# Kernel optimization log

Hardware: AMD Instinct MI355X
Metric: run time of the kernel (lower is better)

## Reference

```python
import jax, jax.numpy as jnp
import numpy as np

EPS = 1e-6


def smooth(p):
    # smooth_distribution: clamp Bernoulli params away from {0,1}
    return jnp.clip(p, EPS, 1.0 - EPS)


def bern_logprob(p, x):
    # Bernoulli(p).log_prob(x) = x*log(p) + (1-x)*log(1-p)
    return x * jnp.log(p) + (1.0 - x) * jnp.log1p(-p)


def binary_row_reduce(A, b, k):
    # GF(2) Gaussian elimination on [A | b]; A:(k,n) binary float, b:(k,)
    M = jnp.concatenate([A, b[:, None]], axis=1)  # (k, n+1)
    rows = jnp.arange(k)
    for i in range(k):  # k is a small static int (25)
        col = M[:, i]
        cand = jnp.where((rows >= i) & (col > 0.5), rows, k)
        p = jnp.minimum(jnp.min(cand), k - 1)  # pivot row (fallback k-1 if none; prob ~0 for random A)
        ri, rp = M[i], M[p]
        M = M.at[i].set(rp)
        M = M.at[p].set(ri)
        elim = (M[:, i] > 0.5) & (rows != i)
        M = jnp.where(elim[:, None], jnp.mod(M + M[i], 2.0), M)
    return M[:, :-1], M[:, -1]


def compute_term1(logq, logp):
    # stable [sum_s q*log p]/[sum_s q], summed over batch; logq,logp: (S,B)
    m = jnp.max(logq, axis=0)                                  # (B,)
    w = jnp.exp(logq - m)                                      # (S,B)
    neg_num = m + jnp.log(jnp.sum(w * (-logp), axis=0))
    pos_den = m + jnp.log(jnp.sum(w, axis=0))
    return -jnp.sum(jnp.exp(neg_num - pos_den))


def setup_inputs() -> dict:
    key = jax.random.key(0)
    ks = jax.random.split(key, 5)
    nx, nz, B = 2048, 256, 512
    wr = float(np.sqrt(6.0 / (nx + nz)))
    xr = float(np.sqrt(6.0 / nx))
    zr = float(np.sqrt(6.0 / nz))
    U = jax.random.uniform(ks[0], (nz, nx), minval=-wr, maxval=wr)
    V = jax.random.uniform(ks[1], (nx, nz), minval=-wr, maxval=wr)
    x_bias = jax.random.uniform(ks[2], (nx,), minval=-xr, maxval=xr)
    z_bias = jax.random.uniform(ks[3], (nz,), minval=-zr, maxval=zr)
    xin = (jax.random.uniform(ks[4], (B, nx)) < 0.5).astype(jnp.float32)
    return {"xin": xin, "U": U, "V": V, "x_bias": x_bias, "z_bias": z_bias,
            "S": 10, "k": 25, "T": 30}


def reference(xin, U, V, x_bias, z_bias, S, k, T):
    dt = xin.dtype
    key = jax.random.key(42)
    kz, kx, kA, kb = jax.random.split(key, 4)

    # q(z|x) and samples  -------------------------------------------------
    q = smooth(jax.nn.sigmoid(xin @ U.T + z_bias))                     # (B, nz)
    samples_z = (jax.random.uniform(kz, (S,) + q.shape) < q).astype(dt)  # (S,B,nz)
    ps = smooth(jax.nn.sigmoid(jnp.einsum('sbz,xz->sbx', samples_z, V) + x_bias))  # (S,B,nx)
    xouts = (jax.random.uniform(kx, ps.shape) < ps).astype(dt)

    # projected ELBO over T random GF(2) hash constraints ------------------
    nz = U.shape[0]
    A_all = (jax.random.uniform(kA, (T, k, nz)) < 0.5).astype(dt)
    b_all = (jax.random.uniform(kb, (T, k)) < 0.5).astype(dt)
    pz = smooth(jax.nn.sigmoid(z_bias))                                # (nz,)

    def elbo_t(carry, Ab):
        A, b = Ab
        C, bp = binary_row_reduce(A, b, k)                             # (k,nz),(k,)
        proj = jnp.mod(jnp.einsum('sbz,kz->sbk', samples_z[:, :, k:], C[:, k:]) + bp, 2.0)
        sz = samples_z.at[:, :, :k].set(proj)                          # (S,B,nz)
        logq_zi = bern_logprob(q, sz).sum(axis=2)                      # (S,B)
        logp_z = bern_logprob(pz, sz).sum(axis=2)                      # (S,B)
        ps_t = smooth(jax.nn.sigmoid(jnp.einsum('sbz,xz->sbx', sz, V) + x_bias))
        logp_x = bern_logprob(ps_t, xin).sum(axis=2)                   # (S,B)
        logp = logp_z + logp_x
        term2 = compute_term1(logq_zi, logq_zi)
        term1 = compute_term1(logq_zi, logp)
        return carry, term1 - term2

    _, pelbos = jax.lax.scan(elbo_t, 0.0, (A_all, b_all))
    loss = -jnp.mean(pelbos)
    return q, samples_z, ps, xouts, loss
```

## Files before the change

### kernel.cpp

```cpp
#include <hip/hip_runtime.h>
#include <cstdint>

#define NX 2048
#define NZ 256
#define NB 512
#define NS 10
#define NK 25
#define NT 30
#define SBTOT (NS * NB)

#define LOG2E 1.4426950408889634f
#define LN2 0.6931471805599453f

#define OFF_Q 0
#define OFF_SAMP (NB * NZ)
#define OFF_PS (OFF_SAMP + SBTOT * NZ)
#define OFF_XO (OFF_PS + SBTOT * NX)
#define OFF_LOSS (OFF_XO + SBTOT * NX)

typedef unsigned long long ull;
typedef __bf16 bf16x8 __attribute__((ext_vector_type(8)));
typedef float f32x4 __attribute__((ext_vector_type(4)));
typedef uint32_t u32x2 __attribute__((ext_vector_type(2)));

__host__ __device__ inline void tf2x32(uint32_t k0, uint32_t k1, uint32_t x0, uint32_t x1,
                                       uint32_t& o0, uint32_t& o1) {
  uint32_t k2 = k0 ^ k1 ^ 0x1BD11BDAu;
  x0 += k0; x1 += k1;
#define TF_R(r) { x0 += x1; x1 = (x1 << (r)) | (x1 >> (32 - (r))); x1 ^= x0; }
  TF_R(13) TF_R(15) TF_R(26) TF_R(6)
  x0 += k1; x1 += k2 + 1u;
  TF_R(17) TF_R(29) TF_R(16) TF_R(24)
  x0 += k2; x1 += k0 + 2u;
  TF_R(13) TF_R(15) TF_R(26) TF_R(6)
  x0 += k0; x1 += k1 + 3u;
  TF_R(17) TF_R(29) TF_R(16) TF_R(24)
  x0 += k1; x1 += k2 + 4u;
  TF_R(13) TF_R(15) TF_R(26) TF_R(6)
  x0 += k2; x1 += k0 + 5u;
#undef TF_R
  o0 = x0; o1 = x1;
}

__device__ inline uint32_t tf_select(uint32_t k0, uint32_t k1, uint32_t i, uint32_t h) {
  bool lo = i < h;
  uint32_t x0 = lo ? i : i - h;
  uint32_t x1 = lo ? i + h : i;
  uint32_t o0, o1;
  tf2x32(k0, k1, x0, x1, o0, o1);
  return lo ? o0 : o1;
}

__device__ inline float tf_uniform(uint32_t k0, uint32_t k1, uint32_t i, uint32_t h) {
  uint32_t r = tf_select(k0, k1, i, h);
  return __uint_as_float(0x3f800000u | (r >> 9)) - 1.0f;
}

__device__ inline float sigclip(float a) {
  float p = 1.0f / (1.0f + __expf(-a));
  return fminf(fmaxf(p, 1e-6f), 1.0f - 1e-6f);
}

__device__ inline ushort f2bf(float f) {
  uint32_t u = __float_as_uint(f);
  return (ushort)((u + 0x7FFFu + ((u >> 16) & 1u)) >> 16);
}

__device__ inline float blockReduceSum256(float v, volatile float* s4) {
#pragma unroll
  for (int o = 32; o > 0; o >>= 1) v += __shfl_down(v, o);
  __syncthreads();
  if ((threadIdx.x & 63) == 0) s4[threadIdx.x >> 6] = v;
  __syncthreads();
  return s4[0] + s4[1] + s4[2] + s4[3];
}

__global__ __launch_bounds__(256) void kP0_prep(const float* __restrict__ V,
                                                const float* __restrict__ U,
                                                const float* __restrict__ xin,
                                                const float* __restrict__ z_bias,
                                                ushort* __restrict__ Vbf,
                                                ushort* __restrict__ Vkpad2,
                                                ushort* __restrict__ Uhi,
                                                ushort* __restrict__ Ulo,
                                                ushort* __restrict__ xinbf,
                                                float* __restrict__ baseq,
                                                float* __restrict__ d_lpz,
                                                float* __restrict__ basepz,
                                                ull* __restrict__ Ct,
                                                uint32_t* __restrict__ bpmask,
                                                uint32_t kA0, uint32_t kA1,
                                                uint32_t kb0, uint32_t kb1) {
  __shared__ float red[4];
  __shared__ uint32_t Aw[NK][8];
  __shared__ uint32_t bbsh[NK];
  int tid = threadIdx.x;
  if (blockIdx.x >= NX * NZ / 256) {
    int t = blockIdx.x - NX * NZ / 256;
    if (tid < NK * 8) {
      int r = tid >> 3, c = tid & 7;
      const uint32_t hA = (uint32_t)NT * NK * NZ / 2;
      uint32_t base_i = (uint32_t)(t * NK + r) * NZ + c * 32;
      uint32_t w = 0;
      for (int zz = 0; zz < 32; ++zz) {
        uint32_t rr = tf_select(kA0, kA1, base_i + zz, hA);
        w |= ((rr >> 31) ^ 1u) << zz;
      }
      Aw[r][c] = w;
    }
    if (tid < NK) {
      const uint32_t hb = (uint32_t)NT * NK / 2;
      uint32_t rb = tf_select(kb0, kb1, (uint32_t)(t * NK + tid), hb);
      bbsh[tid] = (rb >> 31) ^ 1u;
    }
    __syncthreads();
    if (tid >= 64) return;
    int lane = tid;
    ull w0 = 0, w1 = 0, w2 = 0, w3 = 0;
    uint32_t bbit = 0;
    if (lane < NK) {
      w0 = (ull)Aw[lane][0] | ((ull)Aw[lane][1] << 32);
      w1 = (ull)Aw[lane][2] | ((ull)Aw[lane][3] << 32);
      w2 = (ull)Aw[lane][4] | ((ull)Aw[lane][5] << 32);
      w3 = (ull)Aw[lane][6] | ((ull)Aw[lane][7] << 32);
      bbit = bbsh[lane];
    }
    for (int i = 0; i < NK; ++i) {
      int mybit = (int)((w0 >> i) & 1ull);
      ull mask = __ballot(lane < NK && mybit);
      ull cand = mask & (~0ull << i);
      int p = cand ? __builtin_ctzll(cand) : (NK - 1);
      int srcl = (lane == i) ? p : ((lane == p) ? i : lane);
      w0 = __shfl(w0, srcl); w1 = __shfl(w1, srcl); w2 = __shfl(w2, srcl); w3 = __shfl(w3, srcl);
      bbit = __shfl(bbit, srcl);
      ull p0 = __shfl(w0, i), p1 = __shfl(w1, i), p2 = __shfl(w2, i), p3 = __shfl(w3, i);
      uint32_t pvb = __shfl(bbit, i);
      int nb2 = (int)((w0 >> i) & 1ull);
      if (lane < NK && lane != i && nb2) {
        w0 ^= p0; w1 ^= p1; w2 ^= p2; w3 ^= p3; bbit ^= pvb;
      }
    }
    if (lane < NK) {
      w0 &= ~((1ull << NK) - 1ull);
      ull* dstp = Ct + (size_t)(t * NK + lane) * 4;
      dstp[0] = w0; dstp[1] = w1; dstp[2] = w2; dstp[3] = w3;
    }
    ull bm = __ballot(lane < NK && bbit);
    if (lane == 0) bpmask[t] = (uint32_t)bm & 0x1FFFFFFu;
    return;
  }
  int e = blockIdx.x * 256 + tid;
  {
    int x = e >> 8, k = e & 255;
    float v = V[e];
    Vbf[e] = f2bf(v);
    if (k < 32) Vkpad2[x * 32 + k] = (k < NK) ? f2bf(v * LOG2E) : (ushort)0;
  }
  {
    float u = U[e];
    ushort hi = f2bf(u);
    Uhi[e] = hi;
    float hv = __uint_as_float((uint32_t)hi << 16);
    Ulo[e] = f2bf(u - hv);
  }
  {
    xinbf[e] = (xin[e] > 0.5f) ? (ushort)0x3F80 : (ushort)0;
    int e2 = e + NX * NZ;
    xinbf[e2] = (xin[e2] > 0.5f) ? (ushort)0x3F80 : (ushort)0;
  }
  if (e < NB) baseq[e] = 0.0f;
  if (blockIdx.x == 0) {
    int z = tid;
    float pz = sigclip(z_bias[z]);
    float lp = __logf(pz), l1 = __logf(1.0f - pz);
    d_lpz[z] = lp - l1;
    float s = blockReduceSum256(l1, red);
    if (z == 0) *basepz = s;
  }
}

__global__ __launch_bounds__(256) void k1w_mfma(const ushort* __restrict__ xinbf,
                                                const ushort* __restrict__ Uhi,
                                                const ushort* __restrict__ Ulo,
                                                const float* __restrict__ z_bias,
                                                const float* __restrict__ xin,
                                                const ushort* __restrict__ Vkpad2,
                                                float* __restrict__ outq,
                                                float* __restrict__ d_lq,
                                                float* __restrict__ baseq,
                                                float* __restrict__ W) {
  __shared__ float red[4][16][17];
  __shared__ float wred[4][NK];
  int tid = threadIdx.x;
  if (blockIdx.x < 512) {
    int wave = tid >> 6, lane = tid & 63, grp = lane >> 4, col = lane & 15;
    int b0 = (blockIdx.x >> 4) * 16;
    int z0 = (blockIdx.x & 15) * 16;
    f32x4 acc = {0.f, 0.f, 0.f, 0.f};
    const ushort* arow = xinbf + (size_t)(b0 + col) * NX + wave * 512 + grp * 8;
    const ushort* bhr = Uhi + (size_t)(z0 + col) * NX + wave * 512 + grp * 8;
    const ushort* blr = Ulo + (size_t)(z0 + col) * NX + wave * 512 + grp * 8;
#pragma unroll 4
    for (int s = 0; s < 16; ++s) {
      bf16x8 a = *(const bf16x8*)(arow + s * 32);
      bf16x8 bh = *(const bf16x8*)(bhr + s * 32);
      bf16x8 bl = *(const bf16x8*)(blr + s * 32);
      acc = __builtin_amdgcn_mfma_f32_16x16x32_bf16(a, bh, acc, 0, 0, 0);
      acc = __builtin_amdgcn_mfma_f32_16x16x32_bf16(a, bl, acc, 0, 0, 0);
    }
#pragma unroll
    for (int r = 0; r < 4; ++r) red[wave][grp * 4 + r][col] = acc[r];
    __syncthreads();
    int bi = tid >> 4, zi = tid & 15;
    float aa = red[0][bi][zi] + red[1][bi][zi] + red[2][bi][zi] + red[3][bi][zi] + z_bias[z0 + zi];
    int b = b0 + bi, z = z0 + zi;
    float q = sigclip(aa);
    outq[b * NZ + z] = q;
    float lq = __logf(q), l1 = __logf(1.0f - q);
    d_lq[b * NZ + z] = lq - l1;
    float s1 = l1;
#pragma unroll
    for (int o = 1; o < 16; o <<= 1) s1 += __shfl_xor(s1, o);
    if (zi == 0) atomicAdd(&baseq[b], s1);
    return;
  }
  int b = blockIdx.x - 512;
  float acc[NK];
#pragma unroll
  for (int j = 0; j < NK; ++j) acc[j] = 0.0f;
#pragma unroll
  for (int i = 0; i < 8; ++i) {
    int x = i * 256 + tid;
    float s = 1.0f - 2.0f * xin[(size_t)b * NX + x];
    const uint4* vp = (const uint4*)(Vkpad2 + (size_t)x * 32);
    uint4 q0 = vp[0], q1 = vp[1], q2 = vp[2], q3 = vp[3];
    uint32_t w[16] = {q0.x, q0.y, q0.z, q0.w, q1.x, q1.y, q1.z, q1.w,
                      q2.x, q2.y, q2.z, q2.w, q3.x, q3.y, q3.z, q3.w};
#pragma unroll
    for (int j = 0; j < NK; ++j) {
      uint32_t wd = w[j >> 1];
      float v = __uint_as_float((j & 1) ? (wd & 0xFFFF0000u) : (wd << 16));
      acc[j] = fmaf(s, v, acc[j]);
    }
  }
#pragma unroll
  for (int j = 0; j < NK; ++j) {
#pragma unroll
    for (int o = 1; o < 64; o <<= 1) acc[j] += __shfl_xor(acc[j], o);
  }
  if ((tid & 63) == 0) {
#pragma unroll
    for (int j = 0; j < NK; ++j) wred[tid >> 6][j] = acc[j];
  }
  __syncthreads();
  if (tid < NK) W[b * 32 + tid] = wred[0][tid] + wred[1][tid] + wred[2][tid] + wred[3][tid];
}

__global__ __launch_bounds__(256) void k2_samples(const float* __restrict__ q,
                                                  const float* __restrict__ d_lq,
                                                  const float* __restrict__ d_lpz,
                                                  const ull* __restrict__ Ct,
                                                  const uint32_t* __restrict__ bpmask,
                                                  const float* __restrict__ W,
                                                  float* __restrict__ samp_out,
                                                  ushort* __restrict__ samp16,
                                                  ull* __restrict__ Spack,
                                                  float* __restrict__ qtail,
                                                  float* __restrict__ ptail,
                                                  uint32_t* __restrict__ projb,
                                                  float* __restrict__ Syd,
                                                  uint32_t kz0, uint32_t kz1) {
  __shared__ float red[4];
  __shared__ ull sp_sh[4];
  int sb = blockIdx.x;
  int z = threadIdx.x;
  int b = sb & (NB - 1);
  uint32_t i = (uint32_t)sb * NZ + z;
  const uint32_t h = (uint32_t)SBTOT * NZ / 2;
  float u = tf_uniform(kz0, kz1, i, h);
  float qv = q[b * NZ + z];
  int smp = (u < qv) ? 1 : 0;
  __builtin_nontemporal_store((float)smp, samp_out + i);
  samp16[i] = smp ? (ushort)0x3F80 : (ushort)0;
  ull m = __ballot(smp);
  if ((z & 63) == 0) { Spack[sb * 4 + (z >> 6)] = m; sp_sh[z >> 6] = m; }
  float dq = (z >= NK && smp) ? d_lq[b * NZ + z] : 0.0f;
  float dp = (z >= NK && smp) ? d_lpz[z] : 0.0f;
  float sq = blockReduceSum256(dq, red);
  float sp = blockReduceSum256(dp, red);
  if (z == 0) { qtail[sb] = sq; ptail[sb] = sp; }
  if (z < 32) {
    int t = z;
    ull s0 = sp_sh[0], s1 = sp_sh[1], s2 = sp_sh[2], s3 = sp_sh[3];
    uint32_t s25 = (uint32_t)(s0 & 0x1FFFFFFull);
    const float* Wb = W + (size_t)b * 32;
    uint32_t out;
    float syd = 0.0f;
    if (t < NT) {
      uint32_t bp = bpmask[t];
      uint32_t pb = 0;
#pragma unroll
      for (int j = 0; j < NK; ++j) {
        const ull* C = Ct + (size_t)(t * NK + j) * 4;
        int par = __popcll(s0 & C[0]) + __popcll(s1 & C[1]) + __popcll(s2 & C[2]) + __popcll(s3 & C[3]);
        uint32_t bit = ((uint32_t)(par ^ (int)(bp >> j))) & 1u;
        pb |= bit << j;
        int d = (int)bit - (int)((s25 >> j) & 1u);
        syd = fmaf((float)d, Wb[j], syd);
      }
      out = pb;
    } else {
      out = s25;
    }
    projb[sb * 32 + t] = out;
    Syd[sb * 32 + t] = syd;
  }
}

__global__ __launch_bounds__(256) void k3m_gemm(const ushort* __restrict__ samp16,
                                                const ushort* __restrict__ Vbf,
                                                const float* __restrict__ x_bias,
                                                ushort* __restrict__ base2,
                                                float* __restrict__ ps_out,
                                                float* __restrict__ xo_out,
                                                uint32_t kx0, uint32_t kx1) {
  __shared__ __align__(16) char smem[2 * 2112 * 4];
  ushort* As = (ushort*)smem;
  ushort* Bs = (ushort*)(smem + 8192);
  float* Tt = (float*)smem;

  int tid = threadIdx.x;
  int wave = tid >> 6, lane = tid & 63, grp = lane >> 4, col = lane & 15;
  int x0 = blockIdx.x * 128;
  int sb0 = blockIdx.y * 32;
  f32x4 acc[2][4];
#pragma unroll
  for (int mi = 0; mi < 2; ++mi)
#pragma unroll
    for (int ni = 0; ni < 4; ++ni) acc[mi][ni] = (f32x4){0.f, 0.f, 0.f, 0.f};

  for (int k0 = 0; k0 < NZ; k0 += 32) {
    {
      int rowb = tid >> 2, kcb = (tid & 3) << 3;
      int sbrow = (rowb < 32) ? (sb0 + rowb) : (sb0 + 2528 + rowb);
      *(uint4*)&Bs[rowb * 32 + kcb] = *(const uint4*)&samp16[(size_t)sbrow * NZ + k0 + kcb];
#pragma unroll
      for (int c = tid; c < 512; c += 256) {
        int rowa = c >> 2, kca = (c & 3) << 3;
        *(uint4*)&As[rowa * 32 + kca] = *(const uint4*)&Vbf[(size_t)(x0 + rowa) * NZ + k0 + kca];
      }
    }
    __syncthreads();
    bf16x8 af[2], bfv[4];
#pragma unroll
    for (int mi = 0; mi < 2; ++mi)
      af[mi] = *(const bf16x8*)&As[(wave * 32 + mi * 16 + col) * 32 + grp * 8];
#pragma unroll
    for (int ni = 0; ni < 4; ++ni)
      bfv[ni] = *(const bf16x8*)&Bs[(ni * 16 + col) * 32 + grp * 8];
#pragma unroll
    for (int mi = 0; mi < 2; ++mi)
#pragma unroll
      for (int ni = 0; ni < 4; ++ni)
        acc[mi][ni] = __builtin_amdgcn_mfma_f32_16x16x32_bf16(af[mi], bfv[ni], acc[mi][ni], 0, 0, 0);
    __syncthreads();
  }

  const uint32_t HH = (uint32_t)(SBTOT / 2) * (uint32_t)NX;
#pragma unroll
  for (int pi = 0; pi < 2; ++pi) {
    __syncthreads();
#pragma unroll
    for (int mi = 0; mi < 2; ++mi) {
      int cbase = wave * 32 + mi * 16 + grp * 4;
      *(float4*)&Tt[col * 132 + cbase] = *(float4*)&acc[mi][pi];
      *(float4*)&Tt[2112 + col * 132 + cbase] = *(float4*)&acc[mi][pi + 2];
    }
    __syncthreads();
#pragma unroll
    for (int pass = 0; pass < 2; ++pass) {
      int r = pass * 8 + (tid >> 5);
      int c = (tid & 31) * 4;
      float4 t0 = *(float4*)&Tt[r * 132 + c];
      float4 t1 = *(float4*)&Tt[2112 + r * 132 + c];
      float4 xb4 = *(const float4*)(x_bias + x0 + c);
      int sb_a = sb0 + pi * 16 + r;
      size_t off_a = (size_t)sb_a * NX + x0 + c;
      size_t off_b = off_a + (size_t)HH;
      float a0 = t0.x + xb4.x, a1 = t0.y + xb4.y, a2 = t0.z + xb4.z, a3 = t0.w + xb4.w;
      float b0 = t1.x + xb4.x, b1 = t1.y + xb4.y, b2 = t1.z + xb4.z, b3 = t1.w + xb4.w;
      u32x2 bpa, bpb;
      bpa[0] = (uint32_t)f2bf(a0 * LOG2E) | ((uint32_t)f2bf(a1 * LOG2E) << 16);
      bpa[1] = (uint32_t)f2bf(a2 * LOG2E) | ((uint32_t)f2bf(a3 * LOG2E) << 16);
      bpb[0] = (uint32_t)f2bf(b0 * LOG2E) | ((uint32_t)f2bf(b1 * LOG2E) << 16);
      bpb[1] = (uint32_t)f2bf(b2 * LOG2E) | ((uint32_t)f2bf(b3 * LOG2E) << 16);
      *(u32x2*)(base2 + off_a) = bpa;
      *(u32x2*)(base2 + off_b) = bpb;
      f32x4 pva = {sigclip(a0), sigclip(a1), sigclip(a2), sigclip(a3)};
      f32x4 pvb = {sigclip(b0), sigclip(b1), sigclip(b2), sigclip(b3)};
      __builtin_nontemporal_store(pva, (f32x4*)(ps_out + off_a));
      __builtin_nontemporal_store(pvb, (f32x4*)(ps_out + off_b));
      uint32_t fi = (uint32_t)off_a;
      uint32_t r0, r1;
      f32x4 xva, xvb;
      tf2x32(kx0, kx1, fi + 0u, fi + 0u + HH, r0, r1);
      xva[0] = ((__uint_as_float(0x3f800000u | (r0 >> 9)) - 1.0f) < pva[0]) ? 1.0f : 0.0f;
      xvb[0] = ((__uint_as_float(0x3f800000u | (r1 >> 9)) - 1.0f) < pvb[0]) ? 1.0f : 0.0f;
      tf2x32(kx0, kx1, fi + 1u, fi + 1u + HH, r0, r1);
      xva[1] = ((__uint_as_float(0x3f800000u | (r0 >> 9)) - 1.0f) < pva[1]) ? 1.0f : 0.0f;
      xvb[1] = ((__uint_as_float(0x3f800000u | (r1 >> 9)) - 1.0f) < pvb[1]) ? 1.0f : 0.0f;
      tf2x32(kx0, kx1, fi + 2u, fi + 2u + HH, r0, r1);
      xva[2] = ((__uint_as_float(0x3f800000u | (r0 >> 9)) - 1.0f) < pva[2]) ? 1.0f : 0.0f;
      xvb[2] = ((__uint_as_float(0x3f800000u | (r1 >> 9)) - 1.0f) < pvb[2]) ? 1.0f : 0.0f;
      tf2x32(kx0, kx1, fi + 3u, fi + 3u + HH, r0, r1);
      xva[3] = ((__uint_as_float(0x3f800000u | (r0 >> 9)) - 1.0f) < pva[3]) ? 1.0f : 0.0f;
      xvb[3] = ((__uint_as_float(0x3f800000u | (r1 >> 9)) - 1.0f) < pvb[3]) ? 1.0f : 0.0f;
      __builtin_nontemporal_store(xva, (f32x4*)(xo_out + off_a));
      __builtin_nontemporal_store(xvb, (f32x4*)(xo_out + off_b));
    }
  }
}

__global__ __launch_bounds__(256) void k6_mfma(const ushort* __restrict__ base2,
                                               const ushort* __restrict__ Vkpad2,
                                               const float* __restrict__ xin,
                                               const uint32_t* __restrict__ projb,
                                               const ull* __restrict__ Spack,
                                               const float* __restrict__ Syd,
                                               float* __restrict__ logpx) {
  __shared__ float bvsm[NX];
  __shared__ float lsum[4][32];
  __shared__ float red[4];
  int sb = blockIdx.x;
  int b = sb & (NB - 1);
  int tid = threadIdx.x;
  int wave = tid >> 6, lane = tid & 63;
  int grp = lane >> 4, col = lane & 15;
  const uint4* b16p = (const uint4*)(base2 + (size_t)sb * NX);
  const float4* x4p = (const float4*)(xin + (size_t)b * NX);
  float sbacc = 0.0f;
  {
    uint4 bu = b16p[tid];
    float4 xv0 = x4p[tid * 2], xv1 = x4p[tid * 2 + 1];
    uint32_t wds[4] = {bu.x, bu.y, bu.z, bu.w};
    float bv[8];
#pragma unroll
    for (int j = 0; j < 8; ++j) {
      uint32_t wd = wds[j >> 1];
      bv[j] = __uint_as_float((j & 1) ? (wd & 0xFFFF0000u) : (wd << 16));
    }
    float sg[8] = {1.0f - 2.0f * xv0.x, 1.0f - 2.0f * xv0.y, 1.0f - 2.0f * xv0.z,
                   1.0f - 2.0f * xv0.w, 1.0f - 2.0f * xv1.x, 1.0f - 2.0f * xv1.y,
                   1.0f - 2.0f * xv1.z, 1.0f - 2.0f * xv1.w};
#pragma unroll
    for (int j = 0; j < 8; ++j) {
      bvsm[tid * 8 + j] = bv[j];
      sbacc = fmaf(sg[j], bv[j], sbacc);
    }
  }
  float Sb = blockReduceSum256(sbacc, red);
  uint32_t s25 = (uint32_t)(Spack[sb * 4] & 0x1FFFFFFull);
  uint32_t pb0 = projb[sb * 32 + col];
  uint32_t pb1 = projb[sb * 32 + 16 + col];
  bf16x8 a0, a1;
  union { ushort u; __bf16 hh; } cvt;
#pragma unroll
  for (int j = 0; j < 8; ++j) {
    int k = grp * 8 + j;
    int sbit = (int)((s25 >> k) & 1u);
    int d0 = (int)((pb0 >> k) & 1u) - sbit;
    int d1 = (int)((pb1 >> k) & 1u) - sbit;
    cvt.u = (ushort)(d0 == 0 ? 0 : (d0 > 0 ? 0x3F80 : 0xBF80)); a0[j] = cvt.hh;
    cvt.u = (ushort)(d1 == 0 ? 0 : (d1 > 0 ? 0x3F80 : 0xBF80)); a1[j] = cvt.hh;
  }
  float acca[8], pp[8];
#pragma unroll
  for (int r = 0; r < 8; ++r) { acca[r] = 0.0f; pp[r] = 1.0f; }
  const ushort* vkbase = Vkpad2 + (size_t)(wave * 512 + col) * 32 + grp * 8;
#pragma unroll 4
  for (int i = 0; i < 32; ++i) {
    int x = (wave * 32 + i) * 16 + col;
    bf16x8 bfr = *(const bf16x8*)(vkbase + (size_t)i * 16 * 32);
    f32x4 c0 = {0.f, 0.f, 0.f, 0.f}, c1 = {0.f, 0.f, 0.f, 0.f};
    c0 = __builtin_amdgcn_mfma_f32_16x16x32_bf16(a0, bfr, c0, 0, 0, 0);
    c1 = __builtin_amdgcn_mfma_f32_16x16x32_bf16(a1, bfr, c1, 0, 0, 0);
    float bs = bvsm[x];
#pragma unroll
    for (int r = 0; r < 4; ++r) {
      float y0 = bs + c0[r];
      acca[r] += fabsf(y0);
      pp[r] = fmaf(pp[r], __builtin_amdgcn_exp2f(-fabsf(y0)), pp[r]);
      float y1 = bs + c1[r];
      acca[4 + r] += fabsf(y1);
      pp[4 + r] = fmaf(pp[4 + r], __builtin_amdgcn_exp2f(-fabsf(y1)), pp[4 + r]);
    }
  }
#pragma unroll
  for (int r = 0; r < 8; ++r) {
    float m = 0.5f * acca[r] + __log2f(pp[r]);
#pragma unroll
    for (int off = 1; off < 16; off <<= 1) m += __shfl_xor(m, off);
    if (col == 0) {
      int t = (r < 4) ? (grp * 4 + r) : (16 + grp * 4 + (r - 4));
      lsum[wave][t] = m;
    }
  }
  __syncthreads();
  if (tid < NT) {
    float tot = lsum[0][tid] + lsum[1][tid] + lsum[2][tid] + lsum[3][tid];
    tot += 0.5f * (Sb + Syd[sb * 32 + tid]);
    logpx[(size_t)tid * SBTOT + sb] = -LN2 * tot;
  }
}

__global__ __launch_bounds__(64) void k7_reduce(const float* __restrict__ logpx,
                                                const uint32_t* __restrict__ projb,
                                                const float* __restrict__ qtail,
                                                const float* __restrict__ ptail,
                                                const float* __restrict__ baseq,
                                                const float* __restrict__ d_lq,
                                                const float* __restrict__ d_lpz,
                                                const float* __restrict__ basepz,
                                                double* __restrict__ pelbo_part) {
  int t = blockIdx.x;
  int chunk = blockIdx.y;
  int lane = threadIdx.x;
  int b = chunk * 64 + lane;
  float dlq[NK];
#pragma unroll
  for (int j = 0; j < NK; ++j) dlq[j] = d_lq[b * NZ + j];
  float bq = baseq[b];
  float bpz = *basepz;
  float lq[NS], lp[NS];
#pragma unroll
  for (int s = 0; s < NS; ++s) {
    int sb = s * NB + b;
    uint32_t m = projb[sb * 32 + t];
    float sq = 0.0f, spv = 0.0f;
#pragma unroll
    for (int j = 0; j < NK; ++j) {
      float on = (float)((m >> j) & 1u);
      sq += on * dlq[j];
      spv += on * d_lpz[j];
    }
    lq[s] = bq + qtail[sb] + sq;
    lp[s] = logpx[t * SBTOT + sb] + bpz + ptail[sb] + spv;
  }
  float mx = lq[0];
#pragma unroll
  for (int s = 1; s < NS; ++s) mx = fmaxf(mx, lq[s]);
  float den = 0.0f, num = 0.0f;
#pragma unroll
  for (int s = 0; s < NS; ++s) {
    float w = __expf(lq[s] - mx);
    den += w;
    num += w * (lq[s] - lp[s]);
  }
  double v = (double)(num / den);
#pragma unroll
  for (int o = 32; o > 0; o >>= 1) v += __shfl_down(v, o);
  if (lane == 0) pelbo_part[t * 8 + chunk] = v;
}

__global__ __launch_bounds__(64) void k8_loss(const double* __restrict__ pelbo_part,
                                              float* __restrict__ out_loss) {
  int t = threadIdx.x;
  double v = 0.0;
  if (t < NT) {
#pragma unroll
    for (int c = 0; c < 8; ++c) v += pelbo_part[t * 8 + c];
  }
#pragma unroll
  for (int o = 32; o > 0; o >>= 1) v += __shfl_down(v, o);
  if (t == 0) *out_loss = (float)(v / (double)NT);
}

extern "C" void kernel_launch(void* const* d_in, const int* in_sizes, int n_in,
                              void* d_out, int out_size, void* d_ws, size_t ws_size,
                              hipStream_t stream) {
  const float* xin = (const float*)d_in[0];
  const float* U = (const float*)d_in[1];
  const float* V = (const float*)d_in[2];
  const float* x_bias = (const float*)d_in[3];
  const float* z_bias = (const float*)d_in[4];
  float* out = (float*)d_out;

  char* p = (char*)d_ws;
  ushort* base2 = (ushort*)p;             p += (size_t)SBTOT * NX * 2;
  float* d_lq = (float*)p;                p += (size_t)NB * NZ * 4;
  float* baseq = (float*)p;               p += (size_t)NB * 4;
  float* d_lpz = (float*)p;               p += (size_t)NZ * 4;
  float* basepz = (float*)p;              p += 16;
  ull* Spack = (ull*)p;                   p += (size_t)SBTOT * 4 * 8;
  float* qtail = (float*)p;               p += (size_t)SBTOT * 4;
  float* ptail = (float*)p;               p += (size_t)SBTOT * 4;
  ull* Ct = (ull*)p;                      p += (size_t)NT * NK * 4 * 8;
  uint32_t* bpm = (uint32_t*)p;           p += 128;
  uint32_t* projb = (uint32_t*)p;         p += (size_t)SBTOT * 32 * 4;
  float* Syd = (float*)p;                 p += (size_t)SBTOT * 32 * 4;
  float* logpx = (float*)p;               p += (size_t)NT * SBTOT * 4;
  double* pelbo = (double*)p;             p += (size_t)NT * 8 * 8;
  ushort* Vkpad2 = (ushort*)p;            p += (size_t)NX * 32 * 2;
  ushort* Vbf = (ushort*)p;               p += (size_t)NX * NZ * 2;
  ushort* samp16 = (ushort*)p;            p += (size_t)SBTOT * NZ * 2;
  float* W = (float*)p;                   p += (size_t)NB * 32 * 4;
  ushort* Uhi = (ushort*)p;               p += (size_t)NZ * NX * 2;
  ushort* Ulo = (ushort*)p;               p += (size_t)NZ * NX * 2;
  ushort* xinbf = (ushort*)p;             p += (size_t)NB * NX * 2;
  (void)ws_size; (void)in_sizes; (void)n_in; (void)out_size;

  uint32_t o0[4], o1[4];
  for (int j = 0; j < 4; ++j) tf2x32(0u, 42u, (uint32_t)j, (uint32_t)(4 + j), o0[j], o1[j]);
  uint32_t kz0 = o0[0], kz1 = o0[1];
  uint32_t kx0 = o0[2], kx1 = o0[3];
  uint32_t kA0 = o1[0], kA1 = o1[1];
  uint32_t kb0 = o1[2], kb1 = o1[3];

  kP0_prep<<<NX * NZ / 256 + NT, 256, 0, stream>>>(V, U, xin, z_bias, Vbf, Vkpad2,
                                                   Uhi, Ulo, xinbf, baseq, d_lpz, basepz,
                                                   Ct, bpm, kA0, kA1, kb0, kb1);
  k1w_mfma<<<1024, 256, 0, stream>>>(xinbf, Uhi, Ulo, z_bias, xin, Vkpad2,
                                     out + OFF_Q, d_lq, baseq, W);
  k2_samples<<<SBTOT, 256, 0, stream>>>(out + OFF_Q, d_lq, d_lpz, Ct, bpm, W,
                                        out + OFF_SAMP, samp16, Spack, qtail, ptail,
                                        projb, Syd, kz0, kz1);
  dim3 g3(NX / 128, SBTOT / 64);
  k3m_gemm<<<g3, 256, 0, stream>>>(samp16, Vbf, x_bias, base2,
                                   out + OFF_PS, out + OFF_XO, kx0, kx1);
  k6_mfma<<<SBTOT, 256, 0, stream>>>(base2, Vkpad2, xin, projb, Spack, Syd, logpx);
  dim3 g7(NT, 8);
  k7_reduce<<<g7, 64, 0, stream>>>(logpx, projb, qtail, ptail, baseq, d_lq,
                                   d_lpz, basepz, pelbo);
  k8_loss<<<1, 64, 0, stream>>>(pelbo, out + OFF_LOSS);
}
```

Before: 256.7 us.

## Move GF(2) reduction into k1 and fold final loss kernel into reduce via atomics

The per-constraint GF(2) row-reduction blocks move from the prep kernel into the k1 MFMA kernel's grid. The separate final loss kernel is removed: k7 blocks add their partial sums to a double accumulator atomically, and the last block (found through a done counter) writes the loss. In k6, the bias is now preloaded into the MFMA accumulator instead of being added afterward. Together these remove one launch and shorten the tail, at the cost of atomics and a summation order that is no longer deterministic.

After: 254.6 us. Within noise of the previous version (-0.8%).

```diff
diff --git a/kernel.cpp b/kernel.cpp
--- a/kernel.cpp
+++ b/kernel.cpp
@@ -87,16 +87,62 @@
                                                 float* __restrict__ baseq,
                                                 float* __restrict__ d_lpz,
                                                 float* __restrict__ basepz,
+                                                double* __restrict__ loss_acc,
+                                                uint32_t* __restrict__ done_ctr) {
+  __shared__ float red[4];
+  int tid = threadIdx.x;
+  int e = blockIdx.x * 256 + tid;
+  {
+    int x = e >> 8, k = e & 255;
+    float v = V[e];
+    Vbf[e] = f2bf(v);
+    if (k < 32) Vkpad2[x * 32 + k] = (k < NK) ? f2bf(v * LOG2E) : (ushort)0;
+  }
+  {
+    float u = U[e];
+    ushort hi = f2bf(u);
+    Uhi[e] = hi;
+    float hv = __uint_as_float((uint32_t)hi << 16);
+    Ulo[e] = f2bf(u - hv);
+  }
+  {
+    xinbf[e] = (xin[e] > 0.5f) ? (ushort)0x3F80 : (ushort)0;
+    int e2 = e + NX * NZ;
+    xinbf[e2] = (xin[e2] > 0.5f) ? (ushort)0x3F80 : (ushort)0;
+  }
+  if (e < NB) baseq[e] = 0.0f;
+  if (blockIdx.x == 0) {
+    if (tid == 0) { *loss_acc = 0.0; *done_ctr = 0u; }
+    int z = tid;
+    float pz = sigclip(z_bias[z]);
+    float lp = __logf(pz), l1 = __logf(1.0f - pz);
+    d_lpz[z] = lp - l1;
+    float s = blockReduceSum256(l1, red);
+    if (z == 0) *basepz = s;
+  }
+}
+
+__global__ __launch_bounds__(256) void k1w_mfma(const ushort* __restrict__ xinbf,
+                                                const ushort* __restrict__ Uhi,
+                                                const ushort* __restrict__ Ulo,
+                                                const float* __restrict__ z_bias,
+                                                const float* __restrict__ xin,
+                                                const ushort* __restrict__ Vkpad2,
+                                                float* __restrict__ outq,
+                                                float* __restrict__ d_lq,
+                                                float* __restrict__ baseq,
+                                                float* __restrict__ W,
                                                 ull* __restrict__ Ct,
                                                 uint32_t* __restrict__ bpmask,
                                                 uint32_t kA0, uint32_t kA1,
                                                 uint32_t kb0, uint32_t kb1) {
-  __shared__ float red[4];
+  __shared__ float red[4][16][17];
+  __shared__ float wred[4][NK];
   __shared__ uint32_t Aw[NK][8];
   __shared__ uint32_t bbsh[NK];
   int tid = threadIdx.x;
-  if (blockIdx.x >= NX * NZ / 256) {
-    int t = blockIdx.x - NX * NZ / 256;
+  if (blockIdx.x >= 1024) {
+    int t = blockIdx.x - 1024;
     if (tid < NK * 8) {
       int r = tid >> 3, c = tid & 7;
       const uint32_t hA = (uint32_t)NT * NK * NZ / 2;
@@ -149,49 +195,6 @@
     if (lane == 0) bpmask[t] = (uint32_t)bm & 0x1FFFFFFu;
     return;
   }
-  int e = blockIdx.x * 256 + tid;
-  {
-    int x = e >> 8, k = e & 255;
-    float v = V[e];
-    Vbf[e] = f2bf(v);
-    if (k < 32) Vkpad2[x * 32 + k] = (k < NK) ? f2bf(v * LOG2E) : (ushort)0;
-  }
-  {
-    float u = U[e];
-    ushort hi = f2bf(u);
-    Uhi[e] = hi;
-    float hv = __uint_as_float((uint32_t)hi << 16);
-    Ulo[e] = f2bf(u - hv);
-  }
-  {
-    xinbf[e] = (xin[e] > 0.5f) ? (ushort)0x3F80 : (ushort)0;
-    int e2 = e + NX * NZ;
-    xinbf[e2] = (xin[e2] > 0.5f) ? (ushort)0x3F80 : (ushort)0;
-  }
-  if (e < NB) baseq[e] = 0.0f;
-  if (blockIdx.x == 0) {
-    int z = tid;
-    float pz = sigclip(z_bias[z]);
-    float lp = __logf(pz), l1 = __logf(1.0f - pz);
-    d_lpz[z] = lp - l1;
-    float s = blockReduceSum256(l1, red);
-    if (z == 0) *basepz = s;
-  }
-}
-
-__global__ __launch_bounds__(256) void k1w_mfma(const ushort* __restrict__ xinbf,
-                                                const ushort* __restrict__ Uhi,
-                                                const ushort* __restrict__ Ulo,
-                                                const float* __restrict__ z_bias,
-                                                const float* __restrict__ xin,
-                                                const ushort* __restrict__ Vkpad2,
-                                                float* __restrict__ outq,
-                                                float* __restrict__ d_lq,
-                                                float* __restrict__ baseq,
-                                                float* __restrict__ W) {
-  __shared__ float red[4][16][17];
-  __shared__ float wred[4][NK];
-  int tid = threadIdx.x;
   if (blockIdx.x < 512) {
     int wave = tid >> 6, lane = tid & 63, grp = lane >> 4, col = lane & 15;
     int b0 = (blockIdx.x >> 4) * 16;
@@ -477,20 +480,20 @@
 #pragma unroll
   for (int r = 0; r < 8; ++r) { acca[r] = 0.0f; pp[r] = 1.0f; }
   const ushort* vkbase = Vkpad2 + (size_t)(wave * 512 + col) * 32 + grp * 8;
+  const float* bvp = bvsm + wave * 512 + col;
 #pragma unroll 4
   for (int i = 0; i < 32; ++i) {
-    int x = (wave * 32 + i) * 16 + col;
+    float bs = bvp[i * 16];
     bf16x8 bfr = *(const bf16x8*)(vkbase + (size_t)i * 16 * 32);
-    f32x4 c0 = {0.f, 0.f, 0.f, 0.f}, c1 = {0.f, 0.f, 0.f, 0.f};
-    c0 = __builtin_amdgcn_mfma_f32_16x16x32_bf16(a0, bfr, c0, 0, 0, 0);
-    c1 = __builtin_amdgcn_mfma_f32_16x16x32_bf16(a1, bfr, c1, 0, 0, 0);
-    float bs = bvsm[x];
+    f32x4 cb = {bs, bs, bs, bs};
+    f32x4 c0 = __builtin_amdgcn_mfma_f32_16x16x32_bf16(a0, bfr, cb, 0, 0, 0);
+    f32x4 c1 = __builtin_amdgcn_mfma_f32_16x16x32_bf16(a1, bfr, cb, 0, 0, 0);
 #pragma unroll
     for (int r = 0; r < 4; ++r) {
-      float y0 = bs + c0[r];
+      float y0 = c0[r];
       acca[r] += fabsf(y0);
       pp[r] = fmaf(pp[r], __builtin_amdgcn_exp2f(-fabsf(y0)), pp[r]);
-      float y1 = bs + c1[r];
+      float y1 = c1[r];
       acca[4 + r] += fabsf(y1);
       pp[4 + r] = fmaf(pp[4 + r], __builtin_amdgcn_exp2f(-fabsf(y1)), pp[4 + r]);
     }
@@ -521,7 +524,9 @@
                                                 const float* __restrict__ d_lq,
                                                 const float* __restrict__ d_lpz,
                                                 const float* __restrict__ basepz,
-                                                double* __restrict__ pelbo_part) {
+                                                double* __restrict__ loss_acc,
+                                                uint32_t* __restrict__ done_ctr,
+                                                float* __restrict__ out_loss) {
   int t = blockIdx.x;
   int chunk = blockIdx.y;
   int lane = threadIdx.x;
@@ -559,20 +564,15 @@
   double v = (double)(num / den);
 #pragma unroll
   for (int o = 32; o > 0; o >>= 1) v += __shfl_down(v, o);
-  if (lane == 0) pelbo_part[t * 8 + chunk] = v;
-}
-
-__global__ __launch_bounds__(64) void k8_loss(const double* __restrict__ pelbo_part,
-                                              float* __restrict__ out_loss) {
-  int t = threadIdx.x;
-  double v = 0.0;
-  if (t < NT) {
-#pragma unroll
-    for (int c = 0; c < 8; ++c) v += pelbo_part[t * 8 + c];
-  }
-#pragma unroll
-  for (int o = 32; o > 0; o >>= 1) v += __shfl_down(v, o);
-  if (t == 0) *out_loss = (float)(v / (double)NT);
+  if (lane == 0) {
+    atomicAdd(loss_acc, v);
+    __threadfence();
+    uint32_t old = atomicAdd(done_ctr, 1u);
+    if (old == (uint32_t)(NT * 8 - 1)) {
+      double tot = atomicAdd(loss_acc, 0.0);
+      *out_loss = (float)(tot / (double)NT);
+    }
+  }
 }
 
 extern "C" void kernel_launch(void* const* d_in, const int* in_sizes, int n_in,
@@ -599,7 +599,8 @@
   uint32_t* projb = (uint32_t*)p;         p += (size_t)SBTOT * 32 * 4;
   float* Syd = (float*)p;                 p += (size_t)SBTOT * 32 * 4;
   float* logpx = (float*)p;               p += (size_t)NT * SBTOT * 4;
-  double* pelbo = (double*)p;             p += (size_t)NT * 8 * 8;
+  double* loss_acc = (double*)p;          p += 64;
+  uint32_t* done_ctr = (uint32_t*)p;      p += 64;
   ushort* Vkpad2 = (ushort*)p;            p += (size_t)NX * 32 * 2;
   ushort* Vbf = (ushort*)p;               p += (size_t)NX * NZ * 2;
   ushort* samp16 = (ushort*)p;            p += (size_t)SBTOT * NZ * 2;
@@ -616,11 +617,12 @@
   uint32_t kA0 = o1[0], kA1 = o1[1];
   uint32_t kb0 = o1[2], kb1 = o1[3];
 
-  kP0_prep<<<NX * NZ / 256 + NT, 256, 0, stream>>>(V, U, xin, z_bias, Vbf, Vkpad2,
-                                                   Uhi, Ulo, xinbf, baseq, d_lpz, basepz,
-                                                   Ct, bpm, kA0, kA1, kb0, kb1);
-  k1w_mfma<<<1024, 256, 0, stream>>>(xinbf, Uhi, Ulo, z_bias, xin, Vkpad2,
-                                     out + OFF_Q, d_lq, baseq, W);
+  kP0_prep<<<NX * NZ / 256, 256, 0, stream>>>(V, U, xin, z_bias, Vbf, Vkpad2,
+                                              Uhi, Ulo, xinbf, baseq, d_lpz, basepz,
+                                              loss_acc, done_ctr);
+  k1w_mfma<<<1024 + NT, 256, 0, stream>>>(xinbf, Uhi, Ulo, z_bias, xin, Vkpad2,
+                                          out + OFF_Q, d_lq, baseq, W,
+                                          Ct, bpm, kA0, kA1, kb0, kb1);
   k2_samples<<<SBTOT, 256, 0, stream>>>(out + OFF_Q, d_lq, d_lpz, Ct, bpm, W,
                                         out + OFF_SAMP, samp16, Spack, qtail, ptail,
                                         projb, Syd, kz0, kz1);
@@ -630,6 +632,5 @@
   k6_mfma<<<SBTOT, 256, 0, stream>>>(base2, Vkpad2, xin, projb, Spack, Syd, logpx);
   dim3 g7(NT, 8);
   k7_reduce<<<g7, 64, 0, stream>>>(logpx, projb, qtail, ptail, baseq, d_lq,
-                                   d_lpz, basepz, pelbo);
-  k8_loss<<<1, 64, 0, stream>>>(pelbo, out + OFF_LOSS);
-}
+                                   d_lpz, basepz, loss_acc, done_ctr, out + OFF_LOSS);
+}
```
